# Kernel tuning notes

Measured on AMD Instinct MI355X. Metric: run time of the kernel, lower is better.

The kernel has to match this reference:

```python
import jax, jax.numpy as jnp
import numpy as np

B, S, D, H = 4, 2048, 1024, 16
DK = D // H


def setup_inputs() -> dict:
    key = jax.random.key(0)
    ks = jax.random.split(key, 12)
    std = 1.0 / np.sqrt(D)
    return {
        "query": jax.random.normal(ks[0], (B, S, D), jnp.float32),
        "key": jax.random.normal(ks[1], (B, S, D), jnp.float32),
        "value": jax.random.normal(ks[2], (B, S, D), jnp.float32),
        "fc_w": jax.random.normal(ks[3], (D, D), jnp.float32),
        "Wq": jax.random.normal(ks[4], (D, D), jnp.float32) * std,
        "bq": jax.random.normal(ks[5], (D,), jnp.float32) * 0.01,
        "Wk": jax.random.normal(ks[6], (D, D), jnp.float32) * std,
        "bk": jax.random.normal(ks[7], (D,), jnp.float32) * 0.01,
        "Wv": jax.random.normal(ks[8], (D, D), jnp.float32) * std,
        "bv": jax.random.normal(ks[9], (D,), jnp.float32) * 0.01,
        "Wo": jax.random.normal(ks[10], (D, D), jnp.float32) * std,
        "bo": jax.random.normal(ks[11], (D,), jnp.float32) * 0.01,
    }


def reference(query, key, value, fc_w, Wq, bq, Wk, bk, Wv, bv, Wo, bo):
    b = query.shape[0]
    # meta-modulated (scaling) query projection: x @ (fc_w * base_w) + b
    q = jnp.matmul(query, fc_w * Wq) + bq
    k = jnp.matmul(key, Wk) + bk
    v = jnp.matmul(value, Wv) + bv
    # [B, S, D] -> [B, H, S, DK]
    q = q.reshape(b, -1, H, DK).transpose(0, 2, 1, 3)
    k = k.reshape(b, -1, H, DK).transpose(0, 2, 1, 3)
    v = v.reshape(b, -1, H, DK).transpose(0, 2, 1, 3)
    scores = jnp.einsum("bhqd,bhkd->bhqk", q, k) / jnp.sqrt(jnp.float32(DK))
    attn = jax.nn.softmax(scores, axis=-1)  # dropout identity at eval
    x = jnp.einsum("bhqk,bhkd->bhqd", attn, v)
    x = x.transpose(0, 2, 1, 3).reshape(b, -1, H * DK)
    return jnp.matmul(x, Wo) + bo
```

## Files before the change

### kernel.cpp

```cpp
#include <hip/hip_runtime.h>
#include <hip/hip_bf16.h>
#include <stdint.h>

#define BB 4
#define SS 2048
#define DD 1024
#define HH 16
#define DKK 64
#define MT (BB*SS)
#define KK DD

typedef __attribute__((ext_vector_type(8))) short bf16x8;
typedef __attribute__((ext_vector_type(4))) float f32x4;
typedef __attribute__((ext_vector_type(8))) unsigned short u16x8;

__device__ __forceinline__ unsigned short f2bf(float f){
  union { float f; unsigned u; } x; x.f = f;
  unsigned r = x.u + 0x7fffu + ((x.u >> 16) & 1u);
  return (unsigned short)(r >> 16);
}

__device__ __forceinline__ short bfc(float x){
  return (short)__builtin_bit_cast(unsigned short, (__bf16)x);
}

__device__ __forceinline__ float ex2(float x){
#if __has_builtin(__builtin_amdgcn_exp2f)
  return __builtin_amdgcn_exp2f(x);
#else
  return exp2f(x);
#endif
}

__device__ __forceinline__ float fm3(float a, float b, float c){
  return fmaxf(fmaxf(a, b), c);
}

__device__ __forceinline__ void gll16(const void* g, void* l){
  __builtin_amdgcn_global_load_lds(
      (const __attribute__((address_space(1))) void*)g,
      (__attribute__((address_space(3))) void*)l, 16, 0, 0);
}

__global__ __launch_bounds__(256) void cvt_bf16(const float* __restrict__ in,
                                                unsigned short* __restrict__ out){
  int i = blockIdx.x * 256 + threadIdx.x;
  const f32x4* p = (const f32x4*)in;
  f32x4 a = p[2*i], b = p[2*i+1];
  u16x8 o;
  #pragma unroll
  for (int j=0;j<4;j++){ o[j] = f2bf(a[j]); o[4+j] = f2bf(b[j]); }
  ((u16x8*)out)[i] = o;
}

__global__ __launch_bounds__(256) void prep_weights(
    const float* __restrict__ fc, const float* __restrict__ Wq,
    const float* __restrict__ Wk, const float* __restrict__ Wv,
    const float* __restrict__ Wo,
    unsigned short* __restrict__ Wqt, unsigned short* __restrict__ Wkt,
    unsigned short* __restrict__ Wvt, unsigned short* __restrict__ Wot){
  __shared__ float tile[32][33];
  int which = blockIdx.y;
  const float* src = which==0?Wq: which==1?Wk: which==2?Wv:Wo;
  unsigned short* dst = which==0?Wqt: which==1?Wkt: which==2?Wvt:Wot;
  int k0 = (blockIdx.x & 31)*32, n0 = (blockIdx.x >> 5)*32;
  int tid = threadIdx.x;
  #pragma unroll
  for (int i=0;i<4;i++){
    int e = tid + i*256; int r = e>>5, c = e&31;
    float v = src[(size_t)(k0+r)*DD + n0 + c];
    if (which==0) v *= fc[(size_t)(k0+r)*DD + n0 + c];
    tile[r][c] = v;
  }
  __syncthreads();
  #pragma unroll
  for (int i=0;i<4;i++){
    int e = tid + i*256; int r = e>>5, c = e&31;
    dst[(size_t)(n0+r)*DD + k0 + c] = f2bf(tile[c][r]);
  }
}

#define GEMM_BODY(EPI, A, Bt, bias, scale, Cout, m0, n0)                          \
  {                                                                               \
  const int tid = threadIdx.x;                                                    \
  const int lane = tid & 63, wid = tid >> 6;                                      \
  const int wm = wid >> 1, wn = wid & 1;                                          \
  const int g = lane >> 4, lr = lane & 15;                                        \
  f32x4 acc[4][4];                                                                \
  _Pragma("unroll")                                                               \
  for (int i=0;i<4;i++)                                                           \
    _Pragma("unroll")                                                             \
    for (int j=0;j<4;j++) acc[i][j] = (f32x4){0.f,0.f,0.f,0.f};                   \
  const char* gaBase = (const char*)((A)  + (size_t)(m0) * KK);                   \
  const char* gbBase = (const char*)((Bt) + (size_t)(n0) * KK);                   \
  auto stage = [&](int buf, int kt){                                              \
    _Pragma("unroll")                                                             \
    for (int is=0; is<2; ++is){                                                   \
      int t = is*4096 + wid*1024 + lane*16;                                       \
      int row = t >> 6, col = t & 63;                                             \
      gll16(gaBase + (size_t)row*(KK*2) + (size_t)kt*64 + col,                    \
            (char*)&Asb[buf][0] + is*4096 + wid*1024);                            \
      gll16(gbBase + (size_t)row*(KK*2) + (size_t)kt*64 + col,                    \
            (char*)&Bsb[buf][0] + is*4096 + wid*1024);                            \
    }                                                                             \
  };                                                                              \
  stage(0, 0);                                                                    \
  __syncthreads();                                                                \
  int cur = 0;                                                                    \
  for (int kt = 0; kt < KK/32; ++kt){                                             \
    if (kt + 1 < KK/32) stage(cur^1, kt+1);                                       \
    bf16x8 af[4], bfr[4];                                                         \
    _Pragma("unroll")                                                             \
    for (int f=0; f<4; ++f){                                                      \
      int ar = wm*64 + f*16 + lr;                                                 \
      af[f]  = *(const bf16x8*)&Asb[cur][ar*32 + g*8];                            \
      int br = wn*64 + f*16 + lr;                                                 \
      bfr[f] = *(const bf16x8*)&Bsb[cur][br*32 + g*8];                            \
    }                                                                             \
    _Pragma("unroll")                                                             \
    for (int i=0;i<4;i++)                                                         \
      _Pragma("unroll")                                                           \
      for (int j=0;j<4;j++)                                                       \
        acc[i][j] = __builtin_amdgcn_mfma_f32_16x16x32_bf16(af[i], bfr[j], acc[i][j], 0, 0, 0); \
    __syncthreads();                                                              \
    cur ^= 1;                                                                     \
  }                                                                               \
  _Pragma("unroll")                                                               \
  for (int j=0;j<4;j++){                                                          \
    int n = (n0) + wn*64 + j*16 + lr;                                             \
    float bv = (bias)[n];                                                         \
    _Pragma("unroll")                                                             \
    for (int i=0;i<4;i++){                                                        \
      int mbase = (m0) + wm*64 + i*16 + g*4;                                      \
      _Pragma("unroll")                                                           \
      for (int r=0;r<4;r++){                                                      \
        int m = mbase + r;                                                        \
        float v = (acc[i][j][r] + bv) * (scale);                                  \
        if (EPI == 0){                                                            \
          int b = m >> 11, s = m & (SS-1);                                        \
          int h = n >> 6, dk = n & 63;                                            \
          ((unsigned short*)(Cout))[(((size_t)(b*HH + h))*SS + s)*DKK + dk] = f2bf(v); \
        } else {                                                                  \
          ((float*)(Cout))[(size_t)m*DD + n] = v;                                 \
        }                                                                         \
      }                                                                           \
    }                                                                             \
  }                                                                               \
  }

__global__ __launch_bounds__(256) void gemm_qkv(
    const unsigned short* __restrict__ Aq, const unsigned short* __restrict__ Ak,
    const unsigned short* __restrict__ Av,
    const unsigned short* __restrict__ Wq, const unsigned short* __restrict__ Wk,
    const unsigned short* __restrict__ Wv,
    const float* __restrict__ bq, const float* __restrict__ bk,
    const float* __restrict__ bv, float qscale,
    unsigned short* __restrict__ Qo, unsigned short* __restrict__ Ko,
    unsigned short* __restrict__ Vo){
  __shared__ __align__(16) unsigned short Asb[2][128*32];
  __shared__ __align__(16) unsigned short Bsb[2][128*32];
  const int u = blockIdx.x;
  const int which = u % 3, v = u / 3;
  const int xcd = v & 7, jj = v >> 3;
  const int by = xcd*8 + (jj>>3), bx = jj & 7;
  const int m0 = by * 128, n0 = bx * 128;
  const unsigned short* A  = which==0 ? Aq : which==1 ? Ak : Av;
  const unsigned short* Bt = which==0 ? Wq : which==1 ? Wk : Wv;
  const float* bias        = which==0 ? bq : which==1 ? bk : bv;
  unsigned short* C        = which==0 ? Qo : which==1 ? Ko : Vo;
  float scale = which==0 ? qscale : 1.0f;
  GEMM_BODY(0, A, Bt, bias, scale, C, m0, n0)
}

__global__ __launch_bounds__(256) void gemm_o(
    const unsigned short* __restrict__ A, const unsigned short* __restrict__ Bt,
    const float* __restrict__ bias, float* __restrict__ Cout){
  __shared__ __align__(16) unsigned short Asb[2][128*32];
  __shared__ __align__(16) unsigned short Bsb[2][128*32];
  const int sidx = blockIdx.x;
  const int xcd = sidx & 7, jj = sidx >> 3;
  const int by = xcd*8 + (jj>>3), bx = jj & 7;
  const int m0 = by * 128, n0 = bx * 128;
  GEMM_BODY(1, A, Bt, bias, 1.0f, Cout, m0, n0)
}

__global__ __launch_bounds__(256) void transpose_v(const unsigned short* __restrict__ V,
                                                   unsigned short* __restrict__ Vt){
  __shared__ unsigned short t[64][72];
  int bh = blockIdx.y; int s0 = blockIdx.x*64;
  const unsigned short* src = V + ((size_t)bh*SS + s0)*DKK;
  int tid = threadIdx.x;
  #pragma unroll
  for (int i=0;i<2;i++){
    int e = (tid + i*256)*8; int r = e>>6, c = e&63;
    int rp = (r & 35) | ((r & 12) << 1) | ((r & 16) >> 2);
    u16x8 v = *(const u16x8*)(src + (size_t)r*DKK + c);
    #pragma unroll
    for (int j=0;j<8;j++) t[c+j][rp] = v[j];
  }
  __syncthreads();
  unsigned short* dst = Vt + ((size_t)bh*DKK)*SS + s0;
  #pragma unroll
  for (int i=0;i<2;i++){
    int e = (tid + i*256)*8; int d = e>>6, c = e&63;
    u16x8 v = *(const u16x8*)(&t[d][c]);
    *(u16x8*)(dst + (size_t)d*SS + c) = v;
  }
}

__global__ __launch_bounds__(256) void attn(
    const unsigned short* __restrict__ Qg,
    const unsigned short* __restrict__ Kg,
    const unsigned short* __restrict__ Vtg,
    unsigned short* __restrict__ Xg){
  __shared__ __align__(16) unsigned short Ks[2][64*64];
  __shared__ __align__(16) unsigned short Vs[2][64*64];
  const int tid = threadIdx.x;
  const int lane = tid & 63, wid = tid >> 6;
  const int g = lane >> 4, lr = lane & 15;
  const int bh = blockIdx.y;
  const int q0 = blockIdx.x * 128;

  const unsigned short* Qrow = Qg + ((size_t)bh*SS + q0)*DKK;
  const char* Kbase = (const char*)(Kg + (size_t)bh*SS*DKK);
  const char* Vbase = (const char*)(Vtg + (size_t)bh*DKK*SS);

  auto stageK = [&](int buf, int it){
    const char* gk = Kbase + (size_t)it*8192;
    #pragma unroll
    for (int is=0; is<2; ++is){
      int t = is*4096 + wid*1024 + lane*16;
      int row = t >> 7;
      int col = (t & 127) ^ ((row & 7) << 4);
      gll16(gk + row*128 + col, (char*)&Ks[buf][0] + is*4096 + wid*1024);
    }
  };
  auto stageV = [&](int buf, int it){
    #pragma unroll
    for (int is=0; is<2; ++is){
      int t = is*4096 + wid*1024 + lane*16;
      int row = t >> 7;
      int col = (t & 127) ^ ((row & 7) << 4);
      gll16(Vbase + (size_t)row*(SS*2) + (size_t)it*128 + col,
            (char*)&Vs[buf][0] + is*4096 + wid*1024);
    }
  };

  stageK(0, 0); stageV(0, 0);

  bf16x8 qf[2][2];
  #pragma unroll
  for (int u=0; u<2; ++u){
    int qrow = wid*32 + u*16 + lr;
    #pragma unroll
    for (int h2=0; h2<2; ++h2)
      qf[u][h2] = *(const bf16x8*)(Qrow + (size_t)qrow*DKK + g*8 + h2*32);
  }

  f32x4 Xf[2][4];
  #pragma unroll
  for (int u=0; u<2; ++u)
    #pragma unroll
    for (int d=0; d<4; ++d) Xf[u][d] = (f32x4){0.f,0.f,0.f,0.f};
  const f32x4 Zv = (f32x4){0.f,0.f,0.f,0.f};
  float m2[2] = {-1e30f, -1e30f}, ell[2] = {0.f, 0.f};
  const int sw2 = (lr & 7) << 4;

  __syncthreads();

  auto body = [&](int cbuf){
    const char* Kb = (const char*)&Ks[cbuf][0];
    const char* Vb = (const char*)&Vs[cbuf][0];
    f32x4 st[4][2];
    __builtin_amdgcn_s_setprio(1);
    #pragma unroll
    for (int s4=0; s4<4; ++s4){
      int rb = (s4*16 + lr) * 128;
      bf16x8 k0 = *(const bf16x8*)(Kb + rb + ((g*16     ) ^ sw2));
      bf16x8 k1 = *(const bf16x8*)(Kb + rb + ((g*16 + 64) ^ sw2));
      st[s4][0] = __builtin_amdgcn_mfma_f32_16x16x32_bf16(k0, qf[0][0], Zv,        0,0,0);
      st[s4][0] = __builtin_amdgcn_mfma_f32_16x16x32_bf16(k1, qf[0][1], st[s4][0], 0,0,0);
      st[s4][1] = __builtin_amdgcn_mfma_f32_16x16x32_bf16(k0, qf[1][0], Zv,        0,0,0);
      st[s4][1] = __builtin_amdgcn_mfma_f32_16x16x32_bf16(k1, qf[1][1], st[s4][1], 0,0,0);
    }
    __builtin_amdgcn_s_setprio(0);

    bf16x8 pa[2][2];
    #pragma unroll
    for (int u=0; u<2; ++u){
      float t0 = fm3(st[0][u][0], st[0][u][1], st[0][u][2]);
      float t1 = fm3(st[0][u][3], st[1][u][0], st[1][u][1]);
      float t2 = fm3(st[1][u][2], st[1][u][3], st[2][u][0]);
      float t3 = fm3(st[2][u][1], st[2][u][2], st[2][u][3]);
      float t4 = fm3(st[3][u][0], st[3][u][1], st[3][u][2]);
      float tmax = fm3(fm3(t0, t1, t2), fmaxf(t3, t4), st[3][u][3]);
      tmax = fmaxf(tmax, __shfl_xor(tmax, 16));
      tmax = fmaxf(tmax, __shfl_xor(tmax, 32));
      if (__any(tmax > m2[u] + 8.f)){
        float mn = fmaxf(m2[u], tmax);
        float sc = ex2(m2[u] - mn);
        m2[u] = mn;
        ell[u] *= sc;
        #pragma unroll
        for (int r=0; r<4; ++r){
          float scr = __shfl(sc, g*4 + r);
          #pragma unroll
          for (int d=0; d<4; ++d) Xf[u][d][r] *= scr;
        }
      }
      #pragma unroll
      for (int s4=0; s4<4; ++s4)
        #pragma unroll
        for (int r=0; r<4; ++r) st[s4][u][r] = ex2(st[s4][u][r] - m2[u]);
      float ps0 = (st[0][u][0]+st[0][u][1]) + (st[0][u][2]+st[0][u][3]);
      float ps1 = (st[1][u][0]+st[1][u][1]) + (st[1][u][2]+st[1][u][3]);
      float ps2 = (st[2][u][0]+st[2][u][1]) + (st[2][u][2]+st[2][u][3]);
      float ps3 = (st[3][u][0]+st[3][u][1]) + (st[3][u][2]+st[3][u][3]);
      ell[u] += (ps0+ps1) + (ps2+ps3);
      #pragma unroll
      for (int j=0; j<8; ++j){
        pa[u][0][j] = bfc(st[(j>>2)    ][u][j&3]);
        pa[u][1][j] = bfc(st[2 + (j>>2)][u][j&3]);
      }
    }

    __builtin_amdgcn_s_setprio(1);
    #pragma unroll
    for (int d=0; d<4; ++d){
      int rb = (d*16 + lr) * 128;
      bf16x8 b0 = *(const bf16x8*)(Vb + rb + ((g*16     ) ^ sw2));
      bf16x8 b1 = *(const bf16x8*)(Vb + rb + ((g*16 + 64) ^ sw2));
      Xf[0][d] = __builtin_amdgcn_mfma_f32_16x16x32_bf16(pa[0][0], b0, Xf[0][d], 0,0,0);
      Xf[0][d] = __builtin_amdgcn_mfma_f32_16x16x32_bf16(pa[0][1], b1, Xf[0][d], 0,0,0);
      Xf[1][d] = __builtin_amdgcn_mfma_f32_16x16x32_bf16(pa[1][0], b0, Xf[1][d], 0,0,0);
      Xf[1][d] = __builtin_amdgcn_mfma_f32_16x16x32_bf16(pa[1][1], b1, Xf[1][d], 0,0,0);
    }
    __builtin_amdgcn_s_setprio(0);
  };

  for (int it = 0; it < SS/64; it += 2){
    if (it + 1 < SS/64){ stageK(1, it+1); stageV(1, it+1); }
    body(0);
    __syncthreads();
    if (it + 2 < SS/64){ stageK(0, it+2); stageV(0, it+2); }
    body(1);
    __syncthreads();
  }

  int b = bh >> 4, h = bh & 15;
  #pragma unroll
  for (int u=0; u<2; ++u){
    float elt = ell[u];
    elt += __shfl_xor(elt, 16);
    elt += __shfl_xor(elt, 32);
    float rinv[4];
    #pragma unroll
    for (int r=0; r<4; ++r) rinv[r] = 1.0f / __shfl(elt, g*4 + r);
    #pragma unroll
    for (int d=0; d<4; ++d)
      #pragma unroll
      for (int r=0; r<4; ++r){
        int s = q0 + wid*32 + u*16 + g*4 + r;
        int col = h*64 + d*16 + lr;
        Xg[((size_t)b*SS + s)*DD + col] = f2bf(Xf[u][d][r] * rinv[r]);
      }
  }
}

extern "C" void kernel_launch(void* const* d_in, const int* in_sizes, int n_in,
                              void* d_out, int out_size, void* d_ws, size_t ws_size,
                              hipStream_t stream){
  (void)in_sizes; (void)n_in; (void)out_size; (void)ws_size;
  const float* query = (const float*)d_in[0];
  const float* key   = (const float*)d_in[1];
  const float* value = (const float*)d_in[2];
  const float* fc_w  = (const float*)d_in[3];
  const float* Wq    = (const float*)d_in[4];
  const float* bq    = (const float*)d_in[5];
  const float* Wk    = (const float*)d_in[6];
  const float* bk    = (const float*)d_in[7];
  const float* Wv    = (const float*)d_in[8];
  const float* bv    = (const float*)d_in[9];
  const float* Wo    = (const float*)d_in[10];
  const float* bo    = (const float*)d_in[11];

  char* ws = (char*)d_ws;
  const size_t EL = (size_t)BB*SS*DD;
  size_t off = 0;
  auto alloc = [&](size_t bytes){ size_t o = off; off += (bytes + 255) & ~(size_t)255; return o; };
  unsigned short* qb  = (unsigned short*)(ws + alloc(EL*2));
  unsigned short* kb  = (unsigned short*)(ws + alloc(EL*2));
  unsigned short* vb  = (unsigned short*)(ws + alloc(EL*2));
  unsigned short* Wqt = (unsigned short*)(ws + alloc((size_t)DD*DD*2));
  unsigned short* Wkt = (unsigned short*)(ws + alloc((size_t)DD*DD*2));
  unsigned short* Wvt = (unsigned short*)(ws + alloc((size_t)DD*DD*2));
  unsigned short* Wot = (unsigned short*)(ws + alloc((size_t)DD*DD*2));
  unsigned short* Qh  = (unsigned short*)(ws + alloc(EL*2));
  unsigned short* Kh  = (unsigned short*)(ws + alloc(EL*2));
  unsigned short* Vh  = (unsigned short*)(ws + alloc(EL*2));
  unsigned short* Vth = vb;
  unsigned short* Xh  = qb;

  const float SC2 = 0.18033688011112042f;

  const int nbCvt = (int)(EL / 8 / 256);
  cvt_bf16<<<nbCvt, 256, 0, stream>>>(query, qb);
  cvt_bf16<<<nbCvt, 256, 0, stream>>>(key,   kb);
  cvt_bf16<<<nbCvt, 256, 0, stream>>>(value, vb);
  prep_weights<<<dim3(1024, 4), 256, 0, stream>>>(fc_w, Wq, Wk, Wv, Wo, Wqt, Wkt, Wvt, Wot);

  gemm_qkv<<<1536, 256, 0, stream>>>(qb, kb, vb, Wqt, Wkt, Wvt, bq, bk, bv, SC2,
                                     Qh, Kh, Vh);

  transpose_v<<<dim3(SS/64, BB*HH), 256, 0, stream>>>(Vh, Vth);
  attn<<<dim3(SS/128, BB*HH), 256, 0, stream>>>(Qh, Kh, Vth, Xh);

  gemm_o<<<512, 256, 0, stream>>>(Xh, Wot, bo, (float*)d_out);
}
```

Measured before the change: 379.6 us.

## Merge conversion launches, remap attention grid, and pipeline K/V staging with partial waitcnt

The three fp32-to-bf16 conversion launches become a single launch with a y-dimension that selects the tensor. The attention grid is flattened and remapped so that consecutive blocks, grouped by blockIdx mod 8, cover different heads, which may improve cache locality across XCDs. The attention loop swaps __syncthreads for raw s_barrier plus s_waitcnt vmcnt(4), so the next buffer's global-to-LDS loads stay in flight while the current buffer is computed. The exp2 fallback now uses inline v_exp_f32, though the builtin path is normally taken. Manual waitcnt counts risk races if the assumed number of in-flight loads is wrong.

```diff
diff --git a/kernel.cpp b/kernel.cpp
--- a/kernel.cpp
+++ b/kernel.cpp
@@ -28,7 +28,9 @@
 #if __has_builtin(__builtin_amdgcn_exp2f)
   return __builtin_amdgcn_exp2f(x);
 #else
-  return exp2f(x);
+  float r;
+  asm("v_exp_f32 %0, %1" : "=v"(r) : "v"(x));
+  return r;
 #endif
 }
 
@@ -42,8 +44,14 @@
       (__attribute__((address_space(3))) void*)l, 16, 0, 0);
 }
 
-__global__ __launch_bounds__(256) void cvt_bf16(const float* __restrict__ in,
-                                                unsigned short* __restrict__ out){
+__global__ __launch_bounds__(256) void cvt_bf16_3(const float* __restrict__ q,
+                                                  const float* __restrict__ k,
+                                                  const float* __restrict__ v,
+                                                  unsigned short* __restrict__ qo,
+                                                  unsigned short* __restrict__ ko,
+                                                  unsigned short* __restrict__ vo){
+  const float* in = blockIdx.y==0 ? q : blockIdx.y==1 ? k : v;
+  unsigned short* out = blockIdx.y==0 ? qo : blockIdx.y==1 ? ko : vo;
   int i = blockIdx.x * 256 + threadIdx.x;
   const f32x4* p = (const f32x4*)in;
   f32x4 a = p[2*i], b = p[2*i+1];
@@ -218,8 +226,10 @@
   const int tid = threadIdx.x;
   const int lane = tid & 63, wid = tid >> 6;
   const int g = lane >> 4, lr = lane & 15;
-  const int bh = blockIdx.y;
-  const int q0 = blockIdx.x * 128;
+  const int u0 = blockIdx.x;
+  const int wk = (u0 & 7) * 128 + (u0 >> 3);
+  const int bh = wk >> 4;
+  const int q0 = (wk & 15) * 128;
 
   const unsigned short* Qrow = Qg + ((size_t)bh*SS + q0)*DKK;
   const char* Kbase = (const char*)(Kg + (size_t)bh*SS*DKK);
@@ -246,8 +256,6 @@
     }
   };
 
-  stageK(0, 0); stageV(0, 0);
-
   bf16x8 qf[2][2];
   #pragma unroll
   for (int u=0; u<2; ++u){
@@ -256,6 +264,7 @@
     for (int h2=0; h2<2; ++h2)
       qf[u][h2] = *(const bf16x8*)(Qrow + (size_t)qrow*DKK + g*8 + h2*32);
   }
+  stageK(0, 0); stageV(0, 0);
 
   f32x4 Xf[2][4];
   #pragma unroll
@@ -265,8 +274,6 @@
   const f32x4 Zv = (f32x4){0.f,0.f,0.f,0.f};
   float m2[2] = {-1e30f, -1e30f}, ell[2] = {0.f, 0.f};
   const int sw2 = (lr & 7) << 4;
-
-  __syncthreads();
 
   auto body = [&](int cbuf){
     const char* Kb = (const char*)&Ks[cbuf][0];
@@ -339,12 +346,22 @@
   };
 
   for (int it = 0; it < SS/64; it += 2){
-    if (it + 1 < SS/64){ stageK(1, it+1); stageV(1, it+1); }
+    __builtin_amdgcn_s_barrier();
+    stageK(1, it+1); stageV(1, it+1);
+    asm volatile("s_waitcnt vmcnt(4)" ::: "memory");
+    __builtin_amdgcn_s_barrier();
+    __builtin_amdgcn_sched_barrier(0);
     body(0);
-    __syncthreads();
-    if (it + 2 < SS/64){ stageK(0, it+2); stageV(0, it+2); }
+    __builtin_amdgcn_s_barrier();
+    if (it + 2 < SS/64){
+      stageK(0, it+2); stageV(0, it+2);
+      asm volatile("s_waitcnt vmcnt(4)" ::: "memory");
+    } else {
+      asm volatile("s_waitcnt vmcnt(0)" ::: "memory");
+    }
+    __builtin_amdgcn_s_barrier();
+    __builtin_amdgcn_sched_barrier(0);
     body(1);
-    __syncthreads();
   }
 
   int b = bh >> 4, h = bh & 15;
@@ -404,16 +421,14 @@
   const float SC2 = 0.18033688011112042f;
 
   const int nbCvt = (int)(EL / 8 / 256);
-  cvt_bf16<<<nbCvt, 256, 0, stream>>>(query, qb);
-  cvt_bf16<<<nbCvt, 256, 0, stream>>>(key,   kb);
-  cvt_bf16<<<nbCvt, 256, 0, stream>>>(value, vb);
+  cvt_bf16_3<<<dim3(nbCvt, 3), 256, 0, stream>>>(query, key, value, qb, kb, vb);
   prep_weights<<<dim3(1024, 4), 256, 0, stream>>>(fc_w, Wq, Wk, Wv, Wo, Wqt, Wkt, Wvt, Wot);
 
   gemm_qkv<<<1536, 256, 0, stream>>>(qb, kb, vb, Wqt, Wkt, Wvt, bq, bk, bv, SC2,
                                      Qh, Kh, Vh);
 
   transpose_v<<<dim3(SS/64, BB*HH), 256, 0, stream>>>(Vh, Vth);
-  attn<<<dim3(SS/128, BB*HH), 256, 0, stream>>>(Qh, Kh, Vth, Xh);
+  attn<<<dim3(SS/128 * BB*HH), 256, 0, stream>>>(Qh, Kh, Vth, Xh);
 
   gemm_o<<<512, 256, 0, stream>>>(Xh, Wot, bo, (float*)d_out);
 }
```

After: 384.8 us. No clear change (+1.4%).
